# Kernel tuning notes

Hardware: AMD Instinct MI355X
Metric: run time of the kernel (lower is better)

The kernel has to match this reference:

```python
import jax, jax.numpy as jnp
import numpy as np

B, N, HID, H = 2, 2048, 2048, 16
DH = HID // H  # 128


def _rope_tables(n, d, base=10000.0):
    inv_freq = 1.0 / (base ** (np.arange(0, d, 2, dtype=np.float32) / d))
    t = np.arange(n, dtype=np.float32)
    freqs = np.outer(t, inv_freq)                 # [N, d/2]
    emb = np.concatenate([freqs, freqs], axis=-1)  # [N, d]
    return jnp.asarray(np.cos(emb)), jnp.asarray(np.sin(emb))


def setup_inputs() -> dict:
    key = jax.random.key(0)
    k1, k2, k3 = jax.random.split(key, 3)
    std = 1.0 / HID ** 0.5
    cos, sin = _rope_tables(N, DH)
    return {
        "hidden_states": jax.random.normal(k1, (B, N, HID), dtype=jnp.float32),
        "cos": cos,
        "sin": sin,
        "w_qkv": (jax.random.truncated_normal(k2, -2.0, 2.0, (3 * HID, HID), jnp.float32) * std),
        "w_o": (jax.random.truncated_normal(k3, -2.0, 2.0, (HID, HID), jnp.float32) * std),
    }


def _rotate_half(x):
    d = x.shape[-1] // 2
    return jnp.concatenate([-x[..., d:], x[..., :d]], axis=-1)


def reference(hidden_states, cos, sin, w_qkv, w_o):
    b, n, _ = hidden_states.shape
    qkv = (hidden_states @ w_qkv.T).reshape(b, n, 3, H, DH)
    q, k, v = qkv[:, :, 0], qkv[:, :, 1], qkv[:, :, 2]  # [B,N,H,DH]
    c = cos[:, None, :]  # [N,1,DH] broadcasts over heads
    s = sin[:, None, :]
    q = q * c + _rotate_half(q) * s
    k = k * c + _rotate_half(k) * s
    scale = 1.0 / jnp.sqrt(jnp.asarray(DH, q.dtype))
    scores = jnp.einsum("bqhd,bkhd->bhqk", q, k) * scale
    attn = jax.nn.softmax(scores, axis=-1)
    out = jnp.einsum("bhqk,bkhd->bqhd", attn, v).reshape(b, n, HID)
    return out @ w_o.T
```

## Files before the change

### kernel.cpp

```cpp
#include <hip/hip_runtime.h>
#include <math.h>

#define NB 2
#define NN 2048
#define HIDDEN 2048
#define NHEAD 16
#define DHEAD 128

typedef __attribute__((ext_vector_type(8))) short bf16x8;
typedef __attribute__((ext_vector_type(4))) float floatx4;

static __device__ __forceinline__ short f2bf(float f) {
    union { float f; unsigned u; } v; v.f = f;
    unsigned r = v.u + 0x7fffu + ((v.u >> 16) & 1u);
    return (short)(r >> 16);
}
static __device__ __forceinline__ void gload_lds16(const short* g, short* l) {
    __builtin_amdgcn_global_load_lds(
        (const __attribute__((address_space(1))) void*)g,
        (__attribute__((address_space(3))) void*)l, 16, 0, 0);
}

__global__ __launch_bounds__(256) void cast_bf16_3(
    const float* __restrict__ a, const float* __restrict__ b, const float* __restrict__ c,
    short* __restrict__ oa, short* __restrict__ ob, short* __restrict__ oc,
    int n4a, int n4b, int n4c)
{
    int i = blockIdx.x * 256 + threadIdx.x;
    const float* s; short* d; int j;
    if (i < n4a) { s = a; d = oa; j = i; }
    else if (i < n4a + n4b) { s = b; d = ob; j = i - n4a; }
    else if (i < n4a + n4b + n4c) { s = c; d = oc; j = i - n4a - n4b; }
    else return;
    float4 v = ((const float4*)s)[j];
    short4 o;
    o.x = f2bf(v.x); o.y = f2bf(v.y); o.z = f2bf(v.z); o.w = f2bf(v.w);
    ((short4*)d)[j] = o;
}

__global__ __launch_bounds__(512, 2) void gemm_qkv_256x128(
    const short* __restrict__ A, const short* __restrict__ Bw,
    const float* __restrict__ cosT, const float* __restrict__ sinT,
    short* __restrict__ Qp, short* __restrict__ Kp, short* __restrict__ Vtp)
{
    __shared__ __align__(16) short AB[49152];

    const int tid = threadIdx.x;
    const int w = tid >> 6;
    const int l = tid & 63;
    const int quad = l >> 4;
    const int l15 = l & 15;
    const int bn = blockIdx.x * 128;
    const int bm = blockIdx.y * 256;
    const int K = HIDDEN;

    const short* src[6];
    int ldst[6];
#pragma unroll
    for (int ld = 0; ld < 2; ++ld) {
        int chunk = ld * 512 + tid;
        int row = chunk >> 3;
        int j = (chunk & 7) ^ (row & 7);
        int coff = j * 8;
        src[ld]     = A + (size_t)(bm + row) * K + coff;
        src[2 + ld] = A + (size_t)(bm + 128 + row) * K + coff;
        ldst[ld]     = chunk * 16;
        ldst[2 + ld] = 16384 + chunk * 16;
    }
    {
        int row = tid >> 3;
        int j = (tid & 7) ^ (row & 7);
        int coff = j * 8;
        src[4] = Bw + (size_t)(bn + row) * K + coff;
        src[5] = Bw + (size_t)(bn + 64 + row) * K + coff;
        ldst[4] = 32768 + tid * 16;
        ldst[5] = 32768 + 8192 + tid * 16;
    }

    const int xj = l15 & 7;
    const int jq0 = ((0 * 4 + quad) ^ xj) * 16;
    const int jq1 = ((1 * 4 + quad) ^ xj) * 16;
    const int arow = (w * 32 + l15) * 128;
    const int brow = 32768 + l15 * 128;

    floatx4 acc[2][8];
#pragma unroll
    for (int i = 0; i < 2; ++i)
#pragma unroll
        for (int j = 0; j < 8; ++j) acc[i][j] = (floatx4){0.f, 0.f, 0.f, 0.f};

#pragma unroll
    for (int i = 0; i < 6; ++i)
        gload_lds16(src[i], (short*)((char*)AB + ldst[i]));

#define STAGE(i) gload_lds16(src[i] + kpf, (short*)((char*)AB + ldst[i] + so))
#define MFMA(d, x, y) d = __builtin_amdgcn_mfma_f32_16x16x32_bf16(x, y, d, 0, 0, 0)

    const int NT = K / 64;
#pragma unroll 1
    for (int t = 0; t < NT; ++t) {
        const int co = (t & 1) * 49152;
        const int so = co ^ 49152;
        int kpf = (t + 1) * 64;
        if (kpf == K) kpf = 0;

        bf16x8 a[2][2], b[4][2];

        asm volatile("s_waitcnt vmcnt(1)" ::: "memory");
        __builtin_amdgcn_s_barrier();
#pragma unroll
        for (int m = 0; m < 2; ++m) {
            a[m][0] = *(const bf16x8*)((const char*)AB + co + arow + m * 2048 + jq0);
            a[m][1] = *(const bf16x8*)((const char*)AB + co + arow + m * 2048 + jq1);
        }
#pragma unroll
        for (int n = 0; n < 4; ++n) {
            b[n][0] = *(const bf16x8*)((const char*)AB + co + brow + n * 2048 + jq0);
            b[n][1] = *(const bf16x8*)((const char*)AB + co + brow + n * 2048 + jq1);
        }
        STAGE(0); STAGE(1); STAGE(2); STAGE(3); STAGE(4);
        __builtin_amdgcn_s_setprio(1);
#pragma unroll
        for (int m = 0; m < 2; ++m)
#pragma unroll
            for (int n = 0; n < 4; ++n) {
                MFMA(acc[m][n], a[m][0], b[n][0]);
                MFMA(acc[m][n], a[m][1], b[n][1]);
            }
        __builtin_amdgcn_s_setprio(0);

        asm volatile("s_waitcnt vmcnt(5)" ::: "memory");
        __builtin_amdgcn_s_barrier();
#pragma unroll
        for (int n = 0; n < 4; ++n) {
            b[n][0] = *(const bf16x8*)((const char*)AB + co + brow + (4 + n) * 2048 + jq0);
            b[n][1] = *(const bf16x8*)((const char*)AB + co + brow + (4 + n) * 2048 + jq1);
        }
        STAGE(5);
        __builtin_amdgcn_s_setprio(1);
#pragma unroll
        for (int m = 0; m < 2; ++m)
#pragma unroll
            for (int n = 0; n < 4; ++n) {
                MFMA(acc[m][4 + n], a[m][0], b[n][0]);
                MFMA(acc[m][4 + n], a[m][1], b[n][1]);
            }
        __builtin_amdgcn_s_setprio(0);
    }
#undef STAGE
#undef MFMA

    asm volatile("s_waitcnt vmcnt(0)" ::: "memory");

    const int which = bn >> 11;
    const int head = (bn >> 7) & (NHEAD - 1);
    const float qsc = (which == 0) ? 0.12751791525f : 1.0f;

#pragma unroll
    for (int m = 0; m < 2; ++m) {
#pragma unroll
        for (int reg = 0; reg < 4; ++reg) {
            int gm = bm + w * 32 + m * 16 + quad * 4 + reg;
            int b2 = gm >> 11, nseq = gm & (NN - 1);
            int bh = b2 * NHEAD + head;
            if (which == 2) {
#pragma unroll
                for (int n = 0; n < 8; ++n) {
                    int d = n * 16 + l15;
                    Vtp[((size_t)bh * DHEAD + d) * NN + nseq] = f2bf(acc[m][n][reg]);
                }
            } else {
                short* dst = (which == 0 ? Qp : Kp) + ((size_t)bh * NN + nseq) * DHEAD;
#pragma unroll
                for (int p = 0; p < 4; ++p) {
                    int d0 = p * 16 + l15;
                    float c = cosT[(size_t)nseq * DHEAD + d0];
                    float s = sinT[(size_t)nseq * DHEAD + d0];
                    float e0 = acc[m][p][reg];
                    float e1 = acc[m][p + 4][reg];
                    dst[d0]      = f2bf((e0 * c - e1 * s) * qsc);
                    dst[d0 + 64] = f2bf((e1 * c + e0 * s) * qsc);
                }
            }
        }
    }
}

template <int MODE>
__global__ __launch_bounds__(256) void gemm_bf16_nt(
    const short* __restrict__ A, const short* __restrict__ Bw,
    const float* __restrict__ cosT, const float* __restrict__ sinT,
    short* __restrict__ Qp, short* __restrict__ Kp, short* __restrict__ Vtp,
    float* __restrict__ Cp, int M, int N, int K)
{
    __shared__ __align__(16) short AB[1280 * 8];

    const int tid = threadIdx.x;
    const int w = tid >> 6;
    const int l = tid & 63;
    const int quad = l >> 4;
    const int l15 = l & 15;
    const int bm = blockIdx.y * 128;
    const int bn = blockIdx.x * 128;

    const int wm = (w & 1) * 64;
    const int wn2 = w >> 1;

    const short* gptr[5];
    short* lptr[5];
#pragma unroll
    for (int r5 = 0; r5 < 5; ++r5) {
        int s = r5 * 256 + tid;
        int m = (s < 640) ? s : s - 640;
        int row = m / 5;
        int ch = m - row * 5;
        if (ch == 4) ch = 0;
        gptr[r5] = ((s < 640) ? (A + (size_t)(bm + row) * K)
                              : (Bw + (size_t)(bn + row) * K)) + ch * 8;
        lptr[r5] = &AB[s * 8];
    }

    floatx4 acc[4][4];
#pragma unroll
    for (int i = 0; i < 4; ++i)
#pragma unroll
        for (int j = 0; j < 4; ++j) acc[i][j] = (floatx4){0.f, 0.f, 0.f, 0.f};

    for (int k0 = 0; k0 < K; k0 += 32) {
        __syncthreads();
#pragma unroll
        for (int r5 = 0; r5 < 5; ++r5)
            gload_lds16(gptr[r5] + k0, lptr[r5]);
        __syncthreads();

        bf16x8 af[4], bf[4];
#pragma unroll
        for (int i = 0; i < 4; ++i)
            af[i] = *(const bf16x8*)&AB[((wm + i * 16 + l15) * 5 + quad) * 8];
#pragma unroll
        for (int j = 0; j < 4; ++j) {
            int col = wn2 * 32 + (j & 1) * 16 + ((j >> 1) << 6);
            bf[j] = *(const bf16x8*)&AB[(640 + (col + l15) * 5 + quad) * 8];
        }
#pragma unroll
        for (int i = 0; i < 4; ++i)
#pragma unroll
            for (int j = 0; j < 4; ++j)
                acc[i][j] = __builtin_amdgcn_mfma_f32_16x16x32_bf16(af[i], bf[j], acc[i][j], 0, 0, 0);
    }

    if (MODE == 1) {
#pragma unroll
        for (int i = 0; i < 4; ++i) {
#pragma unroll
            for (int reg = 0; reg < 4; ++reg) {
                int row = bm + wm + i * 16 + quad * 4 + reg;
                float* crow = Cp + (size_t)row * N + bn;
#pragma unroll
                for (int j = 0; j < 4; ++j)
                    crow[wn2 * 32 + (j & 1) * 16 + ((j >> 1) << 6) + l15] = acc[i][j][reg];
            }
        }
    } else {
        const int which = bn >> 11;
        const int head = (bn >> 7) & (NHEAD - 1);
        const float qsc = (which == 0) ? 0.12751791525f : 1.0f;
#pragma unroll
        for (int i = 0; i < 4; ++i) {
#pragma unroll
            for (int reg = 0; reg < 4; ++reg) {
                int m = bm + wm + i * 16 + quad * 4 + reg;
                int b = m >> 11, n = m & (NN - 1);
                int bh = b * NHEAD + head;
                if (which == 2) {
#pragma unroll
                    for (int j = 0; j < 4; ++j) {
                        int d = wn2 * 32 + (j & 1) * 16 + ((j >> 1) << 6) + l15;
                        Vtp[((size_t)bh * DHEAD + d) * NN + n] = f2bf(acc[i][j][reg]);
                    }
                } else {
                    short* dst = (which == 0 ? Qp : Kp) + ((size_t)bh * NN + n) * DHEAD;
#pragma unroll
                    for (int j = 0; j < 2; ++j) {
                        int d0 = wn2 * 32 + j * 16 + l15;
                        float c = cosT[(size_t)n * DHEAD + d0];
                        float s = sinT[(size_t)n * DHEAD + d0];
                        float e0 = acc[i][j][reg], e1 = acc[i][j + 2][reg];
                        dst[d0]      = f2bf((e0 * c - e1 * s) * qsc);
                        dst[d0 + 64] = f2bf((e1 * c + e0 * s) * qsc);
                    }
                }
            }
        }
    }
}

__global__ __launch_bounds__(512, 2) void attn_mfma8(
    const short* __restrict__ Qb, const short* __restrict__ Kb,
    const short* __restrict__ Vt, short* __restrict__ AOb)
{
    __shared__ __align__(16) short Ks[2][64 * 128];
    __shared__ __align__(16) short Vs[2][128 * 64];
    __shared__ __align__(16) short Ps[8][32][72];

    const int tid = threadIdx.x;
    const int w = tid >> 6;
    const int l = tid & 63;
    const int quad = l >> 4;
    const int l15 = l & 15;
    const int bh = blockIdx.y;
    const int qt = blockIdx.x * 256;

    const short* Qg = Qb + (size_t)bh * NN * DHEAD;
    const short* Kg = Kb + (size_t)bh * NN * DHEAD;
    const short* Vg = Vt + (size_t)bh * DHEAD * NN;

    bf16x8 qf[2][4];
#pragma unroll
    for (int mi = 0; mi < 2; ++mi) {
        const short* qrow = Qg + (size_t)(qt + w * 32 + mi * 16 + l15) * DHEAD + quad * 8;
#pragma unroll
        for (int kc = 0; kc < 4; ++kc) qf[mi][kc] = *(const bf16x8*)(qrow + kc * 32);
    }

    const short* ksrc[2]; int kdst[2];
    const short* vsrc[2]; int vdst[2];
#pragma unroll
    for (int rr = 0; rr < 2; ++rr) {
        int s = rr * 512 + tid;
        {
            int row = s >> 4;
            int j = (s & 15) ^ (row & 15);
            ksrc[rr] = Kg + (size_t)row * DHEAD + j * 8;
            kdst[rr] = s * 8;
        }
        {
            int row = s >> 3;
            int c = (s & 7) ^ (row & 7);
            vsrc[rr] = Vg + (size_t)row * NN + c * 8;
            vdst[rr] = s * 8;
        }
    }

    floatx4 of[2][8];
#pragma unroll
    for (int mi = 0; mi < 2; ++mi)
#pragma unroll
        for (int dc = 0; dc < 8; ++dc) of[mi][dc] = (floatx4){0.f, 0.f, 0.f, 0.f};
    float ls[2][4] = {{0.f, 0.f, 0.f, 0.f}, {0.f, 0.f, 0.f, 0.f}};

#pragma unroll
    for (int rr = 0; rr < 2; ++rr) {
        gload_lds16(ksrc[rr], &Ks[0][0] + kdst[rr]);
        gload_lds16(vsrc[rr], &Vs[0][0] + vdst[rr]);
    }
    asm volatile("s_waitcnt vmcnt(0)" ::: "memory");
    __builtin_amdgcn_s_barrier();

    int cur = 0;
#pragma unroll 1
    for (int kt = 0; kt < NN; kt += 64) {
        if (kt + 64 < NN) {
            const int nxt = cur ^ 1;
#pragma unroll
            for (int rr = 0; rr < 2; ++rr) {
                gload_lds16(ksrc[rr] + (size_t)(kt + 64) * DHEAD, &Ks[nxt][0] + kdst[rr]);
                gload_lds16(vsrc[rr] + (kt + 64), &Vs[nxt][0] + vdst[rr]);
            }
        }
        const short* kb = &Ks[cur][0];
        const short* vb = &Vs[cur][0];

        floatx4 sf[2][4];
#pragma unroll
        for (int n16 = 0; n16 < 4; ++n16) {
            bf16x8 kf[4];
            const short* kbase = kb + (n16 * 16 + l15) * 128;
#pragma unroll
            for (int kc = 0; kc < 4; ++kc)
                kf[kc] = *(const bf16x8*)&kbase[((4 * kc + quad) ^ l15) * 8];
#pragma unroll
            for (int mi = 0; mi < 2; ++mi) {
                floatx4 acc = (floatx4){0.f, 0.f, 0.f, 0.f};
#pragma unroll
                for (int kc = 0; kc < 4; ++kc)
                    acc = __builtin_amdgcn_mfma_f32_16x16x32_bf16(qf[mi][kc], kf[kc], acc, 0, 0, 0);
                sf[mi][n16] = acc;
            }
        }

#pragma unroll
        for (int mi = 0; mi < 2; ++mi)
#pragma unroll
            for (int n16 = 0; n16 < 4; ++n16)
#pragma unroll
                for (int r = 0; r < 4; ++r) {
                    float p = exp2f(sf[mi][n16][r]);
                    ls[mi][r] += p;
                    Ps[w][mi * 16 + quad * 4 + r][n16 * 16 + l15] = f2bf(p);
                }

        bf16x8 pa[2][2];
#pragma unroll
        for (int mi = 0; mi < 2; ++mi)
#pragma unroll
            for (int kc = 0; kc < 2; ++kc)
                pa[mi][kc] = *(const bf16x8*)&Ps[w][mi * 16 + l15][kc * 32 + quad * 8];

#pragma unroll
        for (int dc = 0; dc < 8; ++dc) {
            int row = dc * 16 + l15;
#pragma unroll
            for (int kc = 0; kc < 2; ++kc) {
                bf16x8 vf = *(const bf16x8*)&vb[row * 64 + (((kc * 4 + quad) ^ (row & 7)) * 8)];
#pragma unroll
                for (int mi = 0; mi < 2; ++mi)
                    of[mi][dc] = __builtin_amdgcn_mfma_f32_16x16x32_bf16(
                                     pa[mi][kc], vf, of[mi][dc], 0, 0, 0);
            }
        }

        asm volatile("s_waitcnt vmcnt(0)" ::: "memory");
        __builtin_amdgcn_s_barrier();
        cur ^= 1;
    }

    const int b = bh >> 4, h = bh & (NHEAD - 1);
#pragma unroll
    for (int mi = 0; mi < 2; ++mi)
#pragma unroll
        for (int r = 0; r < 4; ++r) {
            float s = ls[mi][r];
            s += __shfl_xor(s, 1, 64);
            s += __shfl_xor(s, 2, 64);
            s += __shfl_xor(s, 4, 64);
            s += __shfl_xor(s, 8, 64);
            float inv = 1.0f / s;
            int row = qt + w * 32 + mi * 16 + quad * 4 + r;
            short* dst = AOb + ((size_t)(b * NN + row)) * HIDDEN + h * DHEAD;
#pragma unroll
            for (int dc = 0; dc < 8; ++dc)
                dst[dc * 16 + l15] = f2bf(of[mi][dc][r] * inv);
        }
}

extern "C" void kernel_launch(void* const* d_in, const int* in_sizes, int n_in,
                              void* d_out, int out_size, void* d_ws, size_t ws_size,
                              hipStream_t stream)
{
    const float* hs = (const float*)d_in[0];
    const float* cosT = (const float*)d_in[1];
    const float* sinT = (const float*)d_in[2];
    const float* wqkv = (const float*)d_in[3];
    const float* wo = (const float*)d_in[4];
    float* out = (float*)d_out;

    const size_t N_HS = (size_t)NB * NN * HIDDEN;
    const size_t N_WQ = (size_t)3 * HIDDEN * HIDDEN;
    const size_t N_WO = (size_t)HIDDEN * HIDDEN;
    const size_t SZ = (size_t)NB * NHEAD * NN * DHEAD;

    short* Ahs   = (short*)d_ws;
    short* Wqkvb = Ahs + N_HS;
    short* Wob   = Wqkvb + N_WQ;
    short* Qb    = Wob + N_WO;
    short* Kb    = Qb + SZ;
    short* Vtb   = Kb + SZ;
    short* AOb   = Vtb + SZ;

    {
        int n4a = (int)(N_HS / 4), n4b = (int)(N_WQ / 4), n4c = (int)(N_WO / 4);
        int total = n4a + n4b + n4c;
        cast_bf16_3<<<(total + 255) / 256, 256, 0, stream>>>(
            hs, wqkv, wo, Ahs, Wqkvb, Wob, n4a, n4b, n4c);
    }
    {
        dim3 grid(3 * HIDDEN / 128, NB * NN / 256);
        gemm_qkv_256x128<<<grid, 512, 0, stream>>>(
            Ahs, Wqkvb, cosT, sinT, Qb, Kb, Vtb);
    }
    {
        dim3 grid(NN / 256, NB * NHEAD);
        attn_mfma8<<<grid, 512, 0, stream>>>(Qb, Kb, Vtb, AOb);
    }
    {
        dim3 grid(HIDDEN / 128, NB * NN / 128);
        gemm_bf16_nt<1><<<grid, 256, 0, stream>>>(
            AOb, Wob, nullptr, nullptr, nullptr, nullptr, nullptr, out,
            NB * NN, HIDDEN, HIDDEN);
    }
}
```

Baseline: 409.1 us.

## Replace output projection GEMM with double-buffered 256x128 XOR-swizzled tile kernel

Swaps the generic 128x128 single-buffered output-projection GEMM for a dedicated 256x128 tile kernel with 512 threads. It double-buffers a 64-wide K slice in LDS and issues next-tile async loads between the MFMA phases, using split vmcnt waits. It also uses an XOR swizzle to avoid LDS bank conflicts and raises wave priority around the MFMA blocks. This targets load latency and barrier stalls in the final GEMM, at the cost of 96KB of LDS per block, which limits occupancy.

```diff
diff --git a/kernel.cpp b/kernel.cpp
--- a/kernel.cpp
+++ b/kernel.cpp
@@ -186,111 +186,128 @@
     }
 }
 
-template <int MODE>
-__global__ __launch_bounds__(256) void gemm_bf16_nt(
+__global__ __launch_bounds__(512, 2) void gemm_out_256x128(
     const short* __restrict__ A, const short* __restrict__ Bw,
-    const float* __restrict__ cosT, const float* __restrict__ sinT,
-    short* __restrict__ Qp, short* __restrict__ Kp, short* __restrict__ Vtp,
-    float* __restrict__ Cp, int M, int N, int K)
+    float* __restrict__ Cp)
 {
-    __shared__ __align__(16) short AB[1280 * 8];
+    __shared__ __align__(16) short AB[49152];
 
     const int tid = threadIdx.x;
     const int w = tid >> 6;
     const int l = tid & 63;
     const int quad = l >> 4;
     const int l15 = l & 15;
-    const int bm = blockIdx.y * 128;
     const int bn = blockIdx.x * 128;
-
-    const int wm = (w & 1) * 64;
-    const int wn2 = w >> 1;
-
-    const short* gptr[5];
-    short* lptr[5];
-#pragma unroll
-    for (int r5 = 0; r5 < 5; ++r5) {
-        int s = r5 * 256 + tid;
-        int m = (s < 640) ? s : s - 640;
-        int row = m / 5;
-        int ch = m - row * 5;
-        if (ch == 4) ch = 0;
-        gptr[r5] = ((s < 640) ? (A + (size_t)(bm + row) * K)
-                              : (Bw + (size_t)(bn + row) * K)) + ch * 8;
-        lptr[r5] = &AB[s * 8];
-    }
-
-    floatx4 acc[4][4];
-#pragma unroll
-    for (int i = 0; i < 4; ++i)
-#pragma unroll
-        for (int j = 0; j < 4; ++j) acc[i][j] = (floatx4){0.f, 0.f, 0.f, 0.f};
-
-    for (int k0 = 0; k0 < K; k0 += 32) {
-        __syncthreads();
-#pragma unroll
-        for (int r5 = 0; r5 < 5; ++r5)
-            gload_lds16(gptr[r5] + k0, lptr[r5]);
-        __syncthreads();
-
-        bf16x8 af[4], bf[4];
-#pragma unroll
-        for (int i = 0; i < 4; ++i)
-            af[i] = *(const bf16x8*)&AB[((wm + i * 16 + l15) * 5 + quad) * 8];
-#pragma unroll
-        for (int j = 0; j < 4; ++j) {
-            int col = wn2 * 32 + (j & 1) * 16 + ((j >> 1) << 6);
-            bf[j] = *(const bf16x8*)&AB[(640 + (col + l15) * 5 + quad) * 8];
-        }
-#pragma unroll
-        for (int i = 0; i < 4; ++i)
-#pragma unroll
-            for (int j = 0; j < 4; ++j)
-                acc[i][j] = __builtin_amdgcn_mfma_f32_16x16x32_bf16(af[i], bf[j], acc[i][j], 0, 0, 0);
-    }
-
-    if (MODE == 1) {
-#pragma unroll
-        for (int i = 0; i < 4; ++i) {
-#pragma unroll
-            for (int reg = 0; reg < 4; ++reg) {
-                int row = bm + wm + i * 16 + quad * 4 + reg;
-                float* crow = Cp + (size_t)row * N + bn;
-#pragma unroll
-                for (int j = 0; j < 4; ++j)
-                    crow[wn2 * 32 + (j & 1) * 16 + ((j >> 1) << 6) + l15] = acc[i][j][reg];
-            }
-        }
-    } else {
-        const int which = bn >> 11;
-        const int head = (bn >> 7) & (NHEAD - 1);
-        const float qsc = (which == 0) ? 0.12751791525f : 1.0f;
-#pragma unroll
-        for (int i = 0; i < 4; ++i) {
-#pragma unroll
-            for (int reg = 0; reg < 4; ++reg) {
-                int m = bm + wm + i * 16 + quad * 4 + reg;
-                int b = m >> 11, n = m & (NN - 1);
-                int bh = b * NHEAD + head;
-                if (which == 2) {
-#pragma unroll
-                    for (int j = 0; j < 4; ++j) {
-                        int d = wn2 * 32 + (j & 1) * 16 + ((j >> 1) << 6) + l15;
-                        Vtp[((size_t)bh * DHEAD + d) * NN + n] = f2bf(acc[i][j][reg]);
-                    }
-                } else {
-                    short* dst = (which == 0 ? Qp : Kp) + ((size_t)bh * NN + n) * DHEAD;
-#pragma unroll
-                    for (int j = 0; j < 2; ++j) {
-                        int d0 = wn2 * 32 + j * 16 + l15;
-                        float c = cosT[(size_t)n * DHEAD + d0];
-                        float s = sinT[(size_t)n * DHEAD + d0];
-                        float e0 = acc[i][j][reg], e1 = acc[i][j + 2][reg];
-                        dst[d0]      = f2bf((e0 * c - e1 * s) * qsc);
-                        dst[d0 + 64] = f2bf((e1 * c + e0 * s) * qsc);
-                    }
-                }
-            }
+    const int bm = blockIdx.y * 256;
+    const int K = HIDDEN;
+
+    const short* src[6];
+    int ldst[6];
+#pragma unroll
+    for (int ld = 0; ld < 2; ++ld) {
+        int chunk = ld * 512 + tid;
+        int row = chunk >> 3;
+        int j = (chunk & 7) ^ (row & 7);
+        int coff = j * 8;
+        src[ld]     = A + (size_t)(bm + row) * K + coff;
+        src[2 + ld] = A + (size_t)(bm + 128 + row) * K + coff;
+        ldst[ld]     = chunk * 16;
+        ldst[2 + ld] = 16384 + chunk * 16;
+    }
+    {
+        int row = tid >> 3;
+        int j = (tid & 7) ^ (row & 7);
+        int coff = j * 8;
+        src[4] = Bw + (size_t)(bn + row) * K + coff;
+        src[5] = Bw + (size_t)(bn + 64 + row) * K + coff;
+        ldst[4] = 32768 + tid * 16;
+        ldst[5] = 32768 + 8192 + tid * 16;
+    }
+
+    const int xj = l15 & 7;
+    const int jq0 = ((0 * 4 + quad) ^ xj) * 16;
+    const int jq1 = ((1 * 4 + quad) ^ xj) * 16;
+    const int arow = (w * 32 + l15) * 128;
+    const int brow = 32768 + l15 * 128;
+
+    floatx4 acc[2][8];
+#pragma unroll
+    for (int i = 0; i < 2; ++i)
+#pragma unroll
+        for (int j = 0; j < 8; ++j) acc[i][j] = (floatx4){0.f, 0.f, 0.f, 0.f};
+
+#pragma unroll
+    for (int i = 0; i < 6; ++i)
+        gload_lds16(src[i], (short*)((char*)AB + ldst[i]));
+
+#define STAGE(i) gload_lds16(src[i] + kpf, (short*)((char*)AB + ldst[i] + so))
+#define MFMA(d, x, y) d = __builtin_amdgcn_mfma_f32_16x16x32_bf16(x, y, d, 0, 0, 0)
+
+    const int NT = K / 64;
+#pragma unroll 1
+    for (int t = 0; t < NT; ++t) {
+        const int co = (t & 1) * 49152;
+        const int so = co ^ 49152;
+        int kpf = (t + 1) * 64;
+        if (kpf == K) kpf = 0;
+
+        bf16x8 a[2][2], b[4][2];
+
+        asm volatile("s_waitcnt vmcnt(1)" ::: "memory");
+        __builtin_amdgcn_s_barrier();
+#pragma unroll
+        for (int m = 0; m < 2; ++m) {
+            a[m][0] = *(const bf16x8*)((const char*)AB + co + arow + m * 2048 + jq0);
+            a[m][1] = *(const bf16x8*)((const char*)AB + co + arow + m * 2048 + jq1);
+        }
+#pragma unroll
+        for (int n = 0; n < 4; ++n) {
+            b[n][0] = *(const bf16x8*)((const char*)AB + co + brow + n * 2048 + jq0);
+            b[n][1] = *(const bf16x8*)((const char*)AB + co + brow + n * 2048 + jq1);
+        }
+        STAGE(0); STAGE(1); STAGE(2); STAGE(3); STAGE(4);
+        __builtin_amdgcn_s_setprio(1);
+#pragma unroll
+        for (int m = 0; m < 2; ++m)
+#pragma unroll
+            for (int n = 0; n < 4; ++n) {
+                MFMA(acc[m][n], a[m][0], b[n][0]);
+                MFMA(acc[m][n], a[m][1], b[n][1]);
+            }
+        __builtin_amdgcn_s_setprio(0);
+
+        asm volatile("s_waitcnt vmcnt(5)" ::: "memory");
+        __builtin_amdgcn_s_barrier();
+#pragma unroll
+        for (int n = 0; n < 4; ++n) {
+            b[n][0] = *(const bf16x8*)((const char*)AB + co + brow + (4 + n) * 2048 + jq0);
+            b[n][1] = *(const bf16x8*)((const char*)AB + co + brow + (4 + n) * 2048 + jq1);
+        }
+        STAGE(5);
+        __builtin_amdgcn_s_setprio(1);
+#pragma unroll
+        for (int m = 0; m < 2; ++m)
+#pragma unroll
+            for (int n = 0; n < 4; ++n) {
+                MFMA(acc[m][4 + n], a[m][0], b[n][0]);
+                MFMA(acc[m][4 + n], a[m][1], b[n][1]);
+            }
+        __builtin_amdgcn_s_setprio(0);
+    }
+#undef STAGE
+#undef MFMA
+
+    asm volatile("s_waitcnt vmcnt(0)" ::: "memory");
+
+#pragma unroll
+    for (int m = 0; m < 2; ++m) {
+#pragma unroll
+        for (int reg = 0; reg < 4; ++reg) {
+            int row = bm + w * 32 + m * 16 + quad * 4 + reg;
+            float* crow = Cp + (size_t)row * HIDDEN + bn;
+#pragma unroll
+            for (int n = 0; n < 8; ++n)
+                crow[n * 16 + l15] = acc[m][n][reg];
         }
     }
 }
@@ -484,9 +501,7 @@
         attn_mfma8<<<grid, 512, 0, stream>>>(Qb, Kb, Vtb, AOb);
     }
     {
-        dim3 grid(HIDDEN / 128, NB * NN / 128);
-        gemm_bf16_nt<1><<<grid, 256, 0, stream>>>(
-            AOb, Wob, nullptr, nullptr, nullptr, nullptr, nullptr, out,
-            NB * NN, HIDDEN, HIDDEN);
-    }
-}
+        dim3 grid(HIDDEN / 128, NB * NN / 256);
+        gemm_out_256x128<<<grid, 512, 0, stream>>>(AOb, Wob, out);
+    }
+}
```

Measured after the change: 400.5 us. 2.1% less time.
